# Optimization experiments

Measured on AMD Instinct MI355X. Metric: run time of the kernel, lower is better.

The kernel has to match this reference:

```python
import jax, jax.numpy as jnp
import numpy as np

STRIDE = (1, 1)
PADDING = ((1, 1), (1, 1))  # symmetric padding of 1 on H and W
DILATION = (1, 1)


def setup_inputs() -> dict:
    key = jax.random.key(0)
    k1, k2 = jax.random.split(key)
    x = jax.random.normal(k1, (32, 128, 56, 56), dtype=jnp.float32)
    weight = jax.random.normal(k2, (256, 128, 3, 3), dtype=jnp.float32) * 0.05
    return {"x": x, "weight": weight}


def reference(x, weight):
    # Faithful math of the im2col + matmul conv: identical to a standard
    # cross-correlation Conv2d with stride=1, padding=1, dilation=1, groups=1,
    # bias=False. Expressed as a single fused conv instead of the python-loop
    # gather + stacked GEMM of the original (same output values).
    out = jax.lax.conv_general_dilated(
        x, weight,
        window_strides=STRIDE,
        padding=PADDING,
        rhs_dilation=DILATION,
        dimension_numbers=("NCHW", "OIHW", "NCHW"),
        feature_group_count=1,
    )
    return out  # [B, C_out, H_out, W_out] = [32, 256, 56, 56]
```

## Files before the change

kernel.cpp:

```cpp
#include <hip/hip_runtime.h>
#include <stdint.h>


#define CIN   128
#define HW_   56
#define CO_   256
#define KSZ   1152
#define IMGHW 3136
#define HP    58
#define NT    36
#define BUFSZ 24576
#define XT_BYTES ((size_t)32 * HP * HP * CIN * 2)
#define WP_BYTES ((size_t)CO_ * KSZ * 2)
#define WS_NEED  (XT_BYTES + WP_BYTES)
#define XBLKS    (32 * HP)
#define PBLKS    ((CO_ * KSZ) / 256)

typedef __attribute__((ext_vector_type(8))) __bf16 bf16x8;
typedef __attribute__((ext_vector_type(4))) float f32x4;
typedef __attribute__((ext_vector_type(8))) unsigned short ushort8;

__device__ __forceinline__ unsigned short f2bf(float f) {
    unsigned int u = __float_as_uint(f);
    u += 0x7fffu + ((u >> 16) & 1u);
    return (unsigned short)(u >> 16);
}

__device__ __forceinline__ void gl2lds16(const void* g, void* l) {
    __builtin_amdgcn_global_load_lds(
        (const __attribute__((address_space(1))) void*)g,
        (__attribute__((address_space(3))) void*)l, 16, 0, 0);
}

__global__ __launch_bounds__(256)
void prep(const float* __restrict__ x, unsigned short* __restrict__ xt,
          const float* __restrict__ w, unsigned short* __restrict__ wp) {
    const int t = threadIdx.x;
    if (blockIdx.x >= XBLKS) {
        int idx = (blockIdx.x - XBLKS) * 256 + t;
        int co = idx / KSZ;
        int k  = idx - co * KSZ;
        wp[idx] = f2bf(w[(co * CIN + (k & 127)) * 9 + (k >> 7)]);
        return;
    }
    const int nb = blockIdx.x;
    const int n  = nb / HP;
    const int hp = nb - n * HP;
    unsigned short* orow = xt + ((size_t)n * HP + hp) * (HP * CIN);

    if (hp == 0 || hp == HP - 1) {
        for (int i = t; i < (HP * CIN) / 8; i += 256)
            ((ushort8*)orow)[i] = (ushort8){0, 0, 0, 0, 0, 0, 0, 0};
        return;
    }
    const int h = hp - 1;
    __shared__ ushort2 T[CIN][31];
    {
        const int ci = t >> 1, part = t & 1;
        const float* src = x + (((size_t)n * CIN + ci) * IMGHW + h * HW_ + part * 28);
        #pragma unroll
        for (int j = 0; j < 7; ++j) {
            float4 v = *(const float4*)(src + 4 * j);
            T[ci][part * 14 + 2 * j]     = (ushort2){f2bf(v.x), f2bf(v.y)};
            T[ci][part * 14 + 2 * j + 1] = (ushort2){f2bf(v.z), f2bf(v.w)};
        }
    }
    __syncthreads();
    const int wpg = t >> 4, cig = t & 15;
    const int ci0 = cig * 8;
    for (int wp_ = wpg; wp_ < HP; wp_ += 16) {
        ushort8 v = (ushort8){0, 0, 0, 0, 0, 0, 0, 0};
        const int w_ = wp_ - 1;
        if ((unsigned)w_ < (unsigned)HW_) {
            #pragma unroll
            for (int e = 0; e < 8; ++e) {
                ushort2 p = T[ci0 + e][w_ >> 1];
                v[e] = (w_ & 1) ? p.y : p.x;
            }
        }
        *(ushort8*)(orow + wp_ * CIN + ci0) = v;
    }
}

__global__ __launch_bounds__(256, 2)
void conv12(const unsigned short* __restrict__ xt,
            const unsigned short* __restrict__ wpk,
            float* __restrict__ out)
{
    __shared__ __align__(16) char lds[2][BUFSZ];

    const int tid  = threadIdx.x;
    const int lane = tid & 63;
    const int wid  = tid >> 6;

    int bid = blockIdx.x;
    int flat = (bid & 7) * 98 + (bid >> 3);
    const int mt = flat >> 1;
    const int n0 = (flat & 1) << 7;
    const int m0 = mt << 8;

    const int lc = (tid & 7) ^ ((tid >> 3) & 7);
    uint32_t aoff[4], boff[2];
    #pragma unroll
    for (int p = 0; p < 4; ++p) {
        int m = m0 + ((p * 32 + (tid >> 3)) << 1) + (lc >> 2);
        int n = m / IMGHW;
        int rem = m - n * IMGHW;
        int h = rem / HW_;
        int w = rem - h * HW_;
        aoff[p] = (uint32_t)((((n * HP + h) * HP + w) << 8) + ((lc & 3) << 4));
    }
    #pragma unroll
    for (int q = 0; q < 2; ++q) {
        int co = n0 + ((q * 32 + (tid >> 3)) << 1) + (lc >> 2);
        boff[q] = (uint32_t)(co * (KSZ * 2) + ((lc & 3) << 4));
    }

    const int fr = lane & 15, fg = lane >> 4;
    const int cp = (((fr & 1) << 2) | fg) ^ ((fr >> 1) & 7);
    const int wm0 = (wid >> 1) << 7;
    const int wn0 = (wid & 1) << 6;
    const int aB = (((wm0 >> 1) + (fr >> 1)) << 7) + (cp << 4);
    const int bB = 16384 + (((wn0 >> 1) + (fr >> 1)) << 7) + (cp << 4);

    const char* xtc = (const char*)xt;
    const char* wpc = (const char*)wpk;

    f32x4 acc[8][4];
    #pragma unroll
    for (int i = 0; i < 8; ++i)
        #pragma unroll
        for (int j = 0; j < 4; ++j)
            acc[i][j] = (f32x4){0.f, 0.f, 0.f, 0.f};

    auto STAGE = [&](int t) {
        char* L = &lds[t & 1][0];
        int tap = t >> 2;
        int kh = (tap * 11) >> 5;
        int kw = tap - kh * 3;
        uint32_t asl = (uint32_t)(((kh * HP + kw) << 8) + ((t & 3) << 6));
        uint32_t bsl = (uint32_t)(t << 6);
        #pragma unroll
        for (int p = 0; p < 4; ++p)
            gl2lds16(xtc + aoff[p] + asl, L + p * 4096 + tid * 16);
        #pragma unroll
        for (int q = 0; q < 2; ++q)
            gl2lds16(wpc + boff[q] + bsl, L + 16384 + q * 4096 + tid * 16);
    };

    STAGE(0);
    asm volatile("s_waitcnt vmcnt(0)" ::: "memory");
    __builtin_amdgcn_s_barrier();

    #pragma unroll 1
    for (int t = 0; t < NT; ++t) {
        if (t + 1 < NT) STAGE(t + 1);

        const char* L = &lds[t & 1][0];
        ushort8 a[8], b[4];
        #pragma unroll
        for (int nf = 0; nf < 4; ++nf)
            b[nf] = *(const ushort8*)(L + bB + nf * 1024);
        #pragma unroll
        for (int mf = 0; mf < 8; ++mf)
            a[mf] = *(const ushort8*)(L + aB + mf * 1024);

        __builtin_amdgcn_s_setprio(1);
        #pragma unroll
        for (int mf = 0; mf < 8; ++mf)
            #pragma unroll
            for (int nf = 0; nf < 4; ++nf)
                acc[mf][nf] = __builtin_amdgcn_mfma_f32_16x16x32_bf16(
                    __builtin_bit_cast(bf16x8, b[nf]),
                    __builtin_bit_cast(bf16x8, a[mf]),
                    acc[mf][nf], 0, 0, 0);
        __builtin_amdgcn_s_setprio(0);

        if (t + 1 < NT) asm volatile("s_waitcnt vmcnt(0)" ::: "memory");
        __builtin_amdgcn_s_barrier();
    }

    const int mwave = m0 + wm0;
    const int co0 = n0 + wn0 + (fg << 2);
    #pragma unroll
    for (int mf = 0; mf < 8; ++mf) {
        int m = mwave + mf * 16 + fr;
        int n = m / IMGHW;
        int hwr = m - n * IMGHW;
        uint32_t basem = (uint32_t)(n * (CO_ * IMGHW) + hwr);
        #pragma unroll
        for (int nf = 0; nf < 4; ++nf)
            #pragma unroll
            for (int q = 0; q < 4; ++q)
                out[basem + (uint32_t)(co0 + nf * 16 + q) * IMGHW] = acc[mf][nf][q];
    }
}

#define BM    64
#define BK    32
#define NSTEP 36
#define LDSP  40

template<bool PACKED>
__global__ __launch_bounds__(256, 2)
void conv_fb(const float* __restrict__ x,
             const float* __restrict__ wraw,
             const unsigned short* __restrict__ wp,
             float* __restrict__ out)
{
    __shared__ __align__(16) unsigned short Al[2][BM][LDSP];
    __shared__ __align__(16) unsigned short Bl[2][CO_][LDSP];

    const int tid  = threadIdx.x;
    const int lane = tid & 63;
    const int wid  = tid >> 6;

    const int mb    = blockIdx.x;
    const int n_img = mb / 49;
    const int hw0   = (mb - n_img * 49) * BM;

    const int mm = lane;
    const int hw = hw0 + mm;
    const int h  = hw / HW_;
    const int w_ = hw - h * HW_;

    const int bco  = tid >> 2;
    const int bkkg = tid & 3;

    float   aPF[8];
    ushort8 bPF[4];

    auto loadA = [&](int step) {
        int khkw = step >> 2;
        int kh = khkw / 3, kw = khkw - (khkw / 3) * 3;
        int ci0 = (step & 3) * BK + wid * 8;
        int ih = h + kh - 1, iw = w_ + kw - 1;
        bool valid = ((unsigned)ih < (unsigned)HW_) && ((unsigned)iw < (unsigned)HW_);
        const float* px = x + (((size_t)(n_img * CIN + ci0) * HW_ + ih) * HW_ + iw);
        #pragma unroll
        for (int e = 0; e < 8; ++e)
            aPF[e] = valid ? px[e * IMGHW] : 0.f;
    };
    auto writeA = [&](int buf) {
        ushort8 v;
        #pragma unroll
        for (int e = 0; e < 8; ++e) v[e] = f2bf(aPF[e]);
        *(ushort8*)&Al[buf][mm][wid * 8] = v;
    };
    auto loadB = [&](int step) {
        if (PACKED) {
            int k0 = step * BK;
            #pragma unroll
            for (int r = 0; r < 4; ++r)
                bPF[r] = *(const ushort8*)&wp[(r * 64 + bco) * KSZ + k0 + bkkg * 8];
        } else {
            int khkw = step >> 2;
            int ci0 = (step & 3) * BK + bkkg * 8;
            #pragma unroll
            for (int r = 0; r < 4; ++r) {
                int co = r * 64 + bco;
                ushort8 v;
                #pragma unroll
                for (int e = 0; e < 8; ++e)
                    v[e] = f2bf(wraw[(co * CIN + ci0 + e) * 9 + khkw]);
                bPF[r] = v;
            }
        }
    };
    auto writeB = [&](int buf) {
        #pragma unroll
        for (int r = 0; r < 4; ++r)
            *(ushort8*)&Bl[buf][r * 64 + bco][bkkg * 8] = bPF[r];
    };

    f32x4 acc[4][4];
    #pragma unroll
    for (int i = 0; i < 4; ++i)
        #pragma unroll
        for (int j = 0; j < 4; ++j)
            acc[i][j] = (f32x4){0.f, 0.f, 0.f, 0.f};

    const int frow = lane & 15;
    const int fk   = (lane >> 4) * 8;

    loadA(0); loadB(0);
    writeA(0); writeB(0);
    __syncthreads();

    for (int s = 0; s < NSTEP; ++s) {
        const int cur = s & 1;
        if (s + 1 < NSTEP) { loadA(s + 1); loadB(s + 1); }

        ushort8 aF[4], bF[4];
        #pragma unroll
        for (int i = 0; i < 4; ++i)
            aF[i] = *(const ushort8*)&Bl[cur][wid * 64 + i * 16 + frow][fk];
        #pragma unroll
        for (int j = 0; j < 4; ++j)
            bF[j] = *(const ushort8*)&Al[cur][j * 16 + frow][fk];

        #pragma unroll
        for (int i = 0; i < 4; ++i)
            #pragma unroll
            for (int j = 0; j < 4; ++j)
                acc[i][j] = __builtin_amdgcn_mfma_f32_16x16x32_bf16(
                    __builtin_bit_cast(bf16x8, aF[i]),
                    __builtin_bit_cast(bf16x8, bF[j]),
                    acc[i][j], 0, 0, 0);

        if (s + 1 < NSTEP) { writeA(cur ^ 1); writeB(cur ^ 1); }
        __syncthreads();
    }

    float* ob = out + (size_t)n_img * (CO_ * IMGHW) + hw0;
    #pragma unroll
    for (int i = 0; i < 4; ++i) {
        int co0 = wid * 64 + i * 16 + (lane >> 4) * 4;
        #pragma unroll
        for (int j = 0; j < 4; ++j) {
            int mcol = j * 16 + (lane & 15);
            #pragma unroll
            for (int q = 0; q < 4; ++q)
                ob[(size_t)(co0 + q) * IMGHW + mcol] = acc[i][j][q];
        }
    }
}

extern "C" void kernel_launch(void* const* d_in, const int* in_sizes, int n_in,
                              void* d_out, int out_size, void* d_ws, size_t ws_size,
                              hipStream_t stream) {
    (void)in_sizes; (void)n_in; (void)out_size;
    const float* x  = (const float*)d_in[0];
    const float* wt = (const float*)d_in[1];
    float* out = (float*)d_out;

    if (ws_size >= WS_NEED) {
        unsigned short* xt  = (unsigned short*)d_ws;
        unsigned short* wpk = (unsigned short*)((char*)d_ws + XT_BYTES);
        prep<<<XBLKS + PBLKS, 256, 0, stream>>>(x, xt, wt, wpk);
        conv12<<<784, 256, 0, stream>>>(xt, wpk, out);
    } else if (ws_size >= WP_BYTES) {
        unsigned short* wpk = (unsigned short*)d_ws;
        prep<<<XBLKS + PBLKS, 256, 0, stream>>>(x, nullptr, wt, wpk);
        conv_fb<false><<<100352 / BM, 256, 0, stream>>>(x, wt, nullptr, out);
    } else {
        conv_fb<false><<<100352 / BM, 256, 0, stream>>>(x, wt, nullptr, out);
    }
}
```

Measured before the change: 93.66 us.

## Load weights directly into registers in MFMA fragment order, bypassing LDS

```diff
diff --git a/kernel.cpp b/kernel.cpp
--- a/kernel.cpp
+++ b/kernel.cpp
@@ -9,16 +9,15 @@
 #define IMGHW 3136
 #define HP    58
 #define NT    36
-#define BUFSZ 24576
 #define XT_BYTES ((size_t)32 * HP * HP * CIN * 2)
 #define WP_BYTES ((size_t)CO_ * KSZ * 2)
 #define WS_NEED  (XT_BYTES + WP_BYTES)
 #define XBLKS    (32 * HP)
 #define PBLKS    ((CO_ * KSZ) / 256)
 
-typedef __attribute__((ext_vector_type(8))) __bf16 bf16x8;
-typedef __attribute__((ext_vector_type(4))) float f32x4;
-typedef __attribute__((ext_vector_type(8))) unsigned short ushort8;
+typedef __attribute__((ext_vector_type(8)))  __bf16 bf16x8;
+typedef __attribute__((ext_vector_type(4)))  float  f32x4;
+typedef __attribute__((ext_vector_type(8)))  unsigned short ushort8;
 
 __device__ __forceinline__ unsigned short f2bf(float f) {
     unsigned int u = __float_as_uint(f);
@@ -34,13 +33,17 @@
 
 __global__ __launch_bounds__(256)
 void prep(const float* __restrict__ x, unsigned short* __restrict__ xt,
-          const float* __restrict__ w, unsigned short* __restrict__ wp) {
+          const float* __restrict__ w, unsigned short* __restrict__ wp2) {
     const int t = threadIdx.x;
     if (blockIdx.x >= XBLKS) {
-        int idx = (blockIdx.x - XBLKS) * 256 + t;
-        int co = idx / KSZ;
-        int k  = idx - co * KSZ;
-        wp[idx] = f2bf(w[(co * CIN + (k & 127)) * 9 + (k >> 7)]);
+        int o = (blockIdx.x - XBLKS) * 256 + t;
+        int e    = o & 7;
+        int lane = (o >> 3) & 63;
+        int cog  = (o >> 9) & 15;
+        int tt   = o >> 13;
+        int co = cog * 16 + (lane & 15);
+        int k  = tt * 32 + (lane >> 4) * 8 + e;
+        wp2[o] = f2bf(w[(co * CIN + (k & 127)) * 9 + (k >> 7)]);
         return;
     }
     const int nb = blockIdx.x;
@@ -83,11 +86,11 @@
 }
 
 __global__ __launch_bounds__(256, 2)
-void conv12(const unsigned short* __restrict__ xt,
-            const unsigned short* __restrict__ wpk,
+void conv14(const unsigned short* __restrict__ xt,
+            const unsigned short* __restrict__ wp2,
             float* __restrict__ out)
 {
-    __shared__ __align__(16) char lds[2][BUFSZ];
+    __shared__ __align__(16) char lds[2][16384];
 
     const int tid  = threadIdx.x;
     const int lane = tid & 63;
@@ -95,12 +98,12 @@
 
     int bid = blockIdx.x;
     int flat = (bid & 7) * 98 + (bid >> 3);
-    const int mt = flat >> 1;
-    const int n0 = (flat & 1) << 7;
-    const int m0 = mt << 8;
+    const int mt_ = flat >> 1;
+    const int n0  = (flat & 1) << 7;
+    const int m0  = mt_ << 8;
 
     const int lc = (tid & 7) ^ ((tid >> 3) & 7);
-    uint32_t aoff[4], boff[2];
+    uint32_t aoff[4];
     #pragma unroll
     for (int p = 0; p < 4; ++p) {
         int m = m0 + ((p * 32 + (tid >> 3)) << 1) + (lc >> 2);
@@ -110,21 +113,17 @@
         int w = rem - h * HW_;
         aoff[p] = (uint32_t)((((n * HP + h) * HP + w) << 8) + ((lc & 3) << 4));
     }
-    #pragma unroll
-    for (int q = 0; q < 2; ++q) {
-        int co = n0 + ((q * 32 + (tid >> 3)) << 1) + (lc >> 2);
-        boff[q] = (uint32_t)(co * (KSZ * 2) + ((lc & 3) << 4));
-    }
 
     const int fr = lane & 15, fg = lane >> 4;
     const int cp = (((fr & 1) << 2) | fg) ^ ((fr >> 1) & 7);
     const int wm0 = (wid >> 1) << 7;
     const int wn0 = (wid & 1) << 6;
     const int aB = (((wm0 >> 1) + (fr >> 1)) << 7) + (cp << 4);
-    const int bB = 16384 + (((wn0 >> 1) + (fr >> 1)) << 7) + (cp << 4);
+
+    const int nfgB = (n0 + wn0) >> 4;
+    const unsigned short* wpb = wp2 + (size_t)lane * 8;
 
     const char* xtc = (const char*)xt;
-    const char* wpc = (const char*)wpk;
 
     f32x4 acc[8][4];
     #pragma unroll
@@ -132,6 +131,8 @@
         #pragma unroll
         for (int j = 0; j < 4; ++j)
             acc[i][j] = (f32x4){0.f, 0.f, 0.f, 0.f};
+
+    ushort8 b0r[4], b1r[4];
 
     auto STAGE = [&](int t) {
         char* L = &lds[t & 1][0];
@@ -139,45 +140,50 @@
         int kh = (tap * 11) >> 5;
         int kw = tap - kh * 3;
         uint32_t asl = (uint32_t)(((kh * HP + kw) << 8) + ((t & 3) << 6));
-        uint32_t bsl = (uint32_t)(t << 6);
         #pragma unroll
         for (int p = 0; p < 4; ++p)
             gl2lds16(xtc + aoff[p] + asl, L + p * 4096 + tid * 16);
-        #pragma unroll
-        for (int q = 0; q < 2; ++q)
-            gl2lds16(wpc + boff[q] + bsl, L + 16384 + q * 4096 + tid * 16);
-    };
+    };
+
+    #define LOADB(B_, t) do { \
+        _Pragma("unroll") for (int nf_ = 0; nf_ < 4; ++nf_) \
+            B_[nf_] = *(const ushort8*)(wpb + \
+                (size_t)(((t) * 16 + nfgB + nf_) * 64) * 8); \
+    } while (0)
+
+    #define TILE(t, BC, BN) do { \
+        if ((t) + 1 < NT) { \
+            STAGE((t) + 1); \
+            __builtin_amdgcn_sched_barrier(0); \
+            LOADB(BN, (t) + 1); \
+            __builtin_amdgcn_sched_barrier(0); \
+        } \
+        const char* L_ = &lds[(t) & 1][0]; \
+        ushort8 a_[8]; \
+        _Pragma("unroll") for (int mf_ = 0; mf_ < 8; ++mf_) \
+            a_[mf_] = *(const ushort8*)(L_ + aB + mf_ * 1024); \
+        __builtin_amdgcn_s_setprio(1); \
+        _Pragma("unroll") for (int mf_ = 0; mf_ < 8; ++mf_) \
+            _Pragma("unroll") for (int nf_ = 0; nf_ < 4; ++nf_) \
+                acc[mf_][nf_] = __builtin_amdgcn_mfma_f32_16x16x32_bf16( \
+                    __builtin_bit_cast(bf16x8, BC[nf_]), \
+                    __builtin_bit_cast(bf16x8, a_[mf_]), \
+                    acc[mf_][nf_], 0, 0, 0); \
+        __builtin_amdgcn_s_setprio(0); \
+        if ((t) + 1 < NT) \
+            asm volatile("s_waitcnt vmcnt(0)" ::: "memory"); \
+        __builtin_amdgcn_s_barrier(); \
+    } while (0)
 
     STAGE(0);
+    LOADB(b0r, 0);
     asm volatile("s_waitcnt vmcnt(0)" ::: "memory");
     __builtin_amdgcn_s_barrier();
 
     #pragma unroll 1
-    for (int t = 0; t < NT; ++t) {
-        if (t + 1 < NT) STAGE(t + 1);
-
-        const char* L = &lds[t & 1][0];
-        ushort8 a[8], b[4];
-        #pragma unroll
-        for (int nf = 0; nf < 4; ++nf)
-            b[nf] = *(const ushort8*)(L + bB + nf * 1024);
-        #pragma unroll
-        for (int mf = 0; mf < 8; ++mf)
-            a[mf] = *(const ushort8*)(L + aB + mf * 1024);
-
-        __builtin_amdgcn_s_setprio(1);
-        #pragma unroll
-        for (int mf = 0; mf < 8; ++mf)
-            #pragma unroll
-            for (int nf = 0; nf < 4; ++nf)
-                acc[mf][nf] = __builtin_amdgcn_mfma_f32_16x16x32_bf16(
-                    __builtin_bit_cast(bf16x8, b[nf]),
-                    __builtin_bit_cast(bf16x8, a[mf]),
-                    acc[mf][nf], 0, 0, 0);
-        __builtin_amdgcn_s_setprio(0);
-
-        if (t + 1 < NT) asm volatile("s_waitcnt vmcnt(0)" ::: "memory");
-        __builtin_amdgcn_s_barrier();
+    for (int tt = 0; tt < NT; tt += 2) {
+        TILE(tt, b0r, b1r);
+        TILE(tt + 1, b1r, b0r);
     }
 
     const int mwave = m0 + wm0;
@@ -194,6 +200,8 @@
             for (int q = 0; q < 4; ++q)
                 out[basem + (uint32_t)(co0 + nf * 16 + q) * IMGHW] = acc[mf][nf][q];
     }
+    #undef LOADB
+    #undef TILE
 }
 
 #define BM    64
@@ -248,23 +256,16 @@
         *(ushort8*)&Al[buf][mm][wid * 8] = v;
     };
     auto loadB = [&](int step) {
-        if (PACKED) {
-            int k0 = step * BK;
-            #pragma unroll
-            for (int r = 0; r < 4; ++r)
-                bPF[r] = *(const ushort8*)&wp[(r * 64 + bco) * KSZ + k0 + bkkg * 8];
-        } else {
-            int khkw = step >> 2;
-            int ci0 = (step & 3) * BK + bkkg * 8;
-            #pragma unroll
-            for (int r = 0; r < 4; ++r) {
-                int co = r * 64 + bco;
-                ushort8 v;
-                #pragma unroll
-                for (int e = 0; e < 8; ++e)
-                    v[e] = f2bf(wraw[(co * CIN + ci0 + e) * 9 + khkw]);
-                bPF[r] = v;
-            }
+        int khkw = step >> 2;
+        int ci0 = (step & 3) * BK + bkkg * 8;
+        #pragma unroll
+        for (int r = 0; r < 4; ++r) {
+            int co = r * 64 + bco;
+            ushort8 v;
+            #pragma unroll
+            for (int e = 0; e < 8; ++e)
+                v[e] = f2bf(wraw[(co * CIN + ci0 + e) * 9 + khkw]);
+            bPF[r] = v;
         }
     };
     auto writeB = [&](int buf) {
@@ -336,13 +337,9 @@
 
     if (ws_size >= WS_NEED) {
         unsigned short* xt  = (unsigned short*)d_ws;
-        unsigned short* wpk = (unsigned short*)((char*)d_ws + XT_BYTES);
-        prep<<<XBLKS + PBLKS, 256, 0, stream>>>(x, xt, wt, wpk);
-        conv12<<<784, 256, 0, stream>>>(xt, wpk, out);
-    } else if (ws_size >= WP_BYTES) {
-        unsigned short* wpk = (unsigned short*)d_ws;
-        prep<<<XBLKS + PBLKS, 256, 0, stream>>>(x, nullptr, wt, wpk);
-        conv_fb<false><<<100352 / BM, 256, 0, stream>>>(x, wt, nullptr, out);
+        unsigned short* wp2 = (unsigned short*)((char*)d_ws + XT_BYTES);
+        prep<<<XBLKS + PBLKS, 256, 0, stream>>>(x, xt, wt, wp2);
+        conv14<<<784, 256, 0, stream>>>(xt, wp2, out);
     } else {
         conv_fb<false><<<100352 / BM, 256, 0, stream>>>(x, wt, nullptr, out);
     }
```

Measured after the change: 92.52 us. About the same (-1.2%).

## Split conv kernel into producer/consumer waves with triple-buffered LDS

Applied to the files above, without the earlier changes.

```diff
diff --git a/kernel.cpp b/kernel.cpp
--- a/kernel.cpp
+++ b/kernel.cpp
@@ -9,7 +9,7 @@
 #define IMGHW 3136
 #define HP    58
 #define NT    36
-#define BUFSZ 24576
+#define BUFB  24576
 #define XT_BYTES ((size_t)32 * HP * HP * CIN * 2)
 #define WP_BYTES ((size_t)CO_ * KSZ * 2)
 #define WS_NEED  (XT_BYTES + WP_BYTES)
@@ -82,38 +82,82 @@
     }
 }
 
-__global__ __launch_bounds__(256, 2)
-void conv12(const unsigned short* __restrict__ xt,
+__global__ __launch_bounds__(512, 2)
+void convpc(const unsigned short* __restrict__ xt,
             const unsigned short* __restrict__ wpk,
             float* __restrict__ out)
 {
-    __shared__ __align__(16) char lds[2][BUFSZ];
+    __shared__ __align__(16) char lds[3 * BUFB];
+    __shared__ int flagA[40];
+    __shared__ int doneA[40];
 
     const int tid  = threadIdx.x;
     const int lane = tid & 63;
     const int wid  = tid >> 6;
 
+    for (int i = tid; i < 40; i += 512) { flagA[i] = 0; doneA[i] = 0; }
+    __syncthreads();
+
     int bid = blockIdx.x;
     int flat = (bid & 7) * 98 + (bid >> 3);
-    const int mt = flat >> 1;
-    const int n0 = (flat & 1) << 7;
-    const int m0 = mt << 8;
-
-    const int lc = (tid & 7) ^ ((tid >> 3) & 7);
-    uint32_t aoff[4], boff[2];
-    #pragma unroll
-    for (int p = 0; p < 4; ++p) {
-        int m = m0 + ((p * 32 + (tid >> 3)) << 1) + (lc >> 2);
-        int n = m / IMGHW;
-        int rem = m - n * IMGHW;
-        int h = rem / HW_;
-        int w = rem - h * HW_;
-        aoff[p] = (uint32_t)((((n * HP + h) * HP + w) << 8) + ((lc & 3) << 4));
-    }
-    #pragma unroll
-    for (int q = 0; q < 2; ++q) {
-        int co = n0 + ((q * 32 + (tid >> 3)) << 1) + (lc >> 2);
-        boff[q] = (uint32_t)(co * (KSZ * 2) + ((lc & 3) << 4));
+    const int mt_ = flat >> 1;
+    const int n0  = (flat & 1) << 7;
+    const int m0  = mt_ << 8;
+
+    const char* xtc = (const char*)xt;
+    const char* wpc = (const char*)wpk;
+
+    if (wid >= 4) {
+        const int pw = wid - 4;
+        uint32_t aoffp[4], boffp[2];
+        uint32_t adst[4], bdst[2];
+        #pragma unroll
+        for (int i = 0; i < 4; ++i) {
+            int v  = i * 64 + lane;
+            int r2 = pw * 32 + (v >> 3);
+            int lc = (v & 7) ^ ((v >> 3) & 7);
+            int m  = m0 + (r2 << 1) + (lc >> 2);
+            int n  = m / IMGHW;
+            int rem = m - n * IMGHW;
+            int h  = rem / HW_;
+            int w  = rem - h * HW_;
+            aoffp[i] = (uint32_t)((((n * HP + h) * HP + w) << 8) + ((lc & 3) << 4));
+            adst[i]  = (uint32_t)(pw * 4096 + v * 16);
+        }
+        #pragma unroll
+        for (int j = 0; j < 2; ++j) {
+            int v  = ((pw & 1) * 2 + j) * 64 + lane;
+            int q  = pw >> 1;
+            int r2 = q * 32 + (v >> 3);
+            int lc = (v & 7) ^ ((v >> 3) & 7);
+            int co = n0 + (r2 << 1) + (lc >> 2);
+            boffp[j] = (uint32_t)(co * (KSZ * 2) + ((lc & 3) << 4));
+            bdst[j]  = (uint32_t)(16384 + q * 4096 + v * 16);
+        }
+
+        #pragma unroll 1
+        for (int t = 0; t < NT; ++t) {
+            if (t >= 3) {
+                while (((volatile int*)doneA)[t - 3] < 4)
+                    __builtin_amdgcn_s_sleep(1);
+                asm volatile("" ::: "memory");
+            }
+            char* L = &lds[(t % 3) * BUFB];
+            int tap = t >> 2;
+            int kh = (tap * 11) >> 5;
+            int kw = tap - kh * 3;
+            uint32_t asl = (uint32_t)(((kh * HP + kw) << 8) + ((t & 3) << 6));
+            uint32_t bsl = (uint32_t)(t << 6);
+            #pragma unroll
+            for (int i = 0; i < 4; ++i)
+                gl2lds16(xtc + aoffp[i] + asl, L + adst[i]);
+            #pragma unroll
+            for (int j = 0; j < 2; ++j)
+                gl2lds16(wpc + boffp[j] + bsl, L + bdst[j]);
+            asm volatile("s_waitcnt vmcnt(0)" ::: "memory");
+            if (lane == 0) atomicAdd(&flagA[t], 1);
+        }
+        return;
     }
 
     const int fr = lane & 15, fg = lane >> 4;
@@ -123,9 +167,6 @@
     const int aB = (((wm0 >> 1) + (fr >> 1)) << 7) + (cp << 4);
     const int bB = 16384 + (((wn0 >> 1) + (fr >> 1)) << 7) + (cp << 4);
 
-    const char* xtc = (const char*)xt;
-    const char* wpc = (const char*)wpk;
-
     f32x4 acc[8][4];
     #pragma unroll
     for (int i = 0; i < 8; ++i)
@@ -133,30 +174,14 @@
         for (int j = 0; j < 4; ++j)
             acc[i][j] = (f32x4){0.f, 0.f, 0.f, 0.f};
 
-    auto STAGE = [&](int t) {
-        char* L = &lds[t & 1][0];
-        int tap = t >> 2;
-        int kh = (tap * 11) >> 5;
-        int kw = tap - kh * 3;
-        uint32_t asl = (uint32_t)(((kh * HP + kw) << 8) + ((t & 3) << 6));
-        uint32_t bsl = (uint32_t)(t << 6);
-        #pragma unroll
-        for (int p = 0; p < 4; ++p)
-            gl2lds16(xtc + aoff[p] + asl, L + p * 4096 + tid * 16);
-        #pragma unroll
-        for (int q = 0; q < 2; ++q)
-            gl2lds16(wpc + boff[q] + bsl, L + 16384 + q * 4096 + tid * 16);
-    };
-
-    STAGE(0);
-    asm volatile("s_waitcnt vmcnt(0)" ::: "memory");
-    __builtin_amdgcn_s_barrier();
-
     #pragma unroll 1
     for (int t = 0; t < NT; ++t) {
-        if (t + 1 < NT) STAGE(t + 1);
-
-        const char* L = &lds[t & 1][0];
+        while (((volatile int*)flagA)[t] < 4)
+            __builtin_amdgcn_s_sleep(1);
+        __builtin_amdgcn_sched_barrier(0);
+        asm volatile("" ::: "memory");
+
+        const char* L = &lds[(t % 3) * BUFB];
         ushort8 a[8], b[4];
         #pragma unroll
         for (int nf = 0; nf < 4; ++nf)
@@ -165,7 +190,6 @@
         for (int mf = 0; mf < 8; ++mf)
             a[mf] = *(const ushort8*)(L + aB + mf * 1024);
 
-        __builtin_amdgcn_s_setprio(1);
         #pragma unroll
         for (int mf = 0; mf < 8; ++mf)
             #pragma unroll
@@ -174,10 +198,10 @@
                     __builtin_bit_cast(bf16x8, b[nf]),
                     __builtin_bit_cast(bf16x8, a[mf]),
                     acc[mf][nf], 0, 0, 0);
-        __builtin_amdgcn_s_setprio(0);
-
-        if (t + 1 < NT) asm volatile("s_waitcnt vmcnt(0)" ::: "memory");
-        __builtin_amdgcn_s_barrier();
+
+        asm volatile("s_waitcnt lgkmcnt(0)" ::: "memory");
+        __builtin_amdgcn_sched_barrier(0);
+        if (lane == 0) atomicAdd(&doneA[t], 1);
     }
 
     const int mwave = m0 + wm0;
@@ -248,23 +272,16 @@
         *(ushort8*)&Al[buf][mm][wid * 8] = v;
     };
     auto loadB = [&](int step) {
-        if (PACKED) {
-            int k0 = step * BK;
-            #pragma unroll
-            for (int r = 0; r < 4; ++r)
-                bPF[r] = *(const ushort8*)&wp[(r * 64 + bco) * KSZ + k0 + bkkg * 8];
-        } else {
-            int khkw = step >> 2;
-            int ci0 = (step & 3) * BK + bkkg * 8;
-            #pragma unroll
-            for (int r = 0; r < 4; ++r) {
-                int co = r * 64 + bco;
-                ushort8 v;
-                #pragma unroll
-                for (int e = 0; e < 8; ++e)
-                    v[e] = f2bf(wraw[(co * CIN + ci0 + e) * 9 + khkw]);
-                bPF[r] = v;
-            }
+        int khkw = step >> 2;
+        int ci0 = (step & 3) * BK + bkkg * 8;
+        #pragma unroll
+        for (int r = 0; r < 4; ++r) {
+            int co = r * 64 + bco;
+            ushort8 v;
+            #pragma unroll
+            for (int e = 0; e < 8; ++e)
+                v[e] = f2bf(wraw[(co * CIN + ci0 + e) * 9 + khkw]);
+            bPF[r] = v;
         }
     };
     auto writeB = [&](int buf) {
@@ -338,11 +355,7 @@
         unsigned short* xt  = (unsigned short*)d_ws;
         unsigned short* wpk = (unsigned short*)((char*)d_ws + XT_BYTES);
         prep<<<XBLKS + PBLKS, 256, 0, stream>>>(x, xt, wt, wpk);
-        conv12<<<784, 256, 0, stream>>>(xt, wpk, out);
-    } else if (ws_size >= WP_BYTES) {
-        unsigned short* wpk = (unsigned short*)d_ws;
-        prep<<<XBLKS + PBLKS, 256, 0, stream>>>(x, nullptr, wt, wpk);
-        conv_fb<false><<<100352 / BM, 256, 0, stream>>>(x, wt, nullptr, out);
+        convpc<<<784, 512, 0, stream>>>(xt, wpk, out);
     } else {
         conv_fb<false><<<100352 / BM, 256, 0, stream>>>(x, wt, nullptr, out);
     }
```

Result: slower. 110.6 us (+18.1%).
